# Performance work log

Measured on AMD Instinct MI355X. Metric: run time of the kernel, lower is better.

Reference implementation:

```python
import jax, jax.numpy as jnp
import numpy as np

QW, KW = 64, 128          # atom query / key window sizes
PAD = (KW - QW) // 2      # halo on each side of the key window
DEPTH, HEADS = 3, 4

def ln(x):
    m = jnp.mean(x, -1, keepdims=True)
    v = jnp.var(x, -1, keepdims=True)
    return (x - m) * jax.lax.rsqrt(v + 1e-5)

def q_windows(x):
    # x: (B, N, ...) -> (B, n, QW, ...); N assumed multiple of QW
    B, N = x.shape[0], x.shape[1]
    n = N // QW
    return x.reshape((B, n, QW) + x.shape[2:])

def k_windows(x):
    # x: (B, N, ...) -> (B, n, KW, ...) sliding key windows with zero halo padding
    B, N = x.shape[0], x.shape[1]
    n = N // QW
    pad_cfg = [(0, 0), (PAD, n * QW + PAD - N)] + [(0, 0)] * (x.ndim - 2)
    xp = jnp.pad(x, pad_cfg)
    idx = jnp.arange(n)[:, None] * QW + jnp.arange(KW)[None, :]
    return xp[:, idx]


def setup_inputs() -> dict:
    key = jax.random.key(0)
    ks = jax.random.split(key, 24)
    B, N, DS, DP, DT, NT = 2, 8192, 128, 16, 384, 1024
    w = lambda k, shp: (jax.random.normal(k, shp, jnp.float32) / np.sqrt(shp[-2])).astype(jnp.float32)
    inp = {
        'ref_pos': jax.random.normal(ks[0], (B, N, 3), jnp.float32),
        'ref_charge': jax.random.normal(ks[1], (B, N, 1), jnp.float32),
        'ref_mask': jnp.ones((B, N, 1), jnp.float32),
        'ref_element': jax.random.uniform(ks[2], (B, N, 128), jnp.float32),
        'ref_atom_name_chars': jax.random.uniform(ks[3], (B, N, 256), jnp.float32),
        'W_single': w(ks[4], (389, DS)),
        'W_pair': w(ks[5], (5, DP)),
        'W_outer': w(ks[6], (DS, 2 * DP)),
        'Wp_ff1': w(ks[7], (DP, 4 * DP)),
        'Wp_ff2': w(ks[8], (4 * DP, DP)),
        'Wq': w(ks[9], (DEPTH, DS, DS)),
        'Wk': w(ks[10], (DEPTH, DS, DS)),
        'Wv': w(ks[11], (DEPTH, DS, DS)),
        'Wo': w(ks[12], (DEPTH, DS, DS)),
        'Wb': w(ks[13], (DP, HEADS)),
        'Wff1': w(ks[14], (DEPTH, DS, 4 * DS)),
        'Wff2': w(ks[15], (DEPTH, 4 * DS, DS)),
        'W_out': w(ks[16], (DS, DT)),
        'ref_space_uid': jnp.sort(jax.random.randint(ks[17], (B, N), 0, NT), axis=-1),
        'atom_to_token_idx': jnp.sort(jax.random.randint(ks[18], (B, N), 0, NT), axis=-1),
        'n_tokens': NT,
    }
    return inp


def reference(ref_pos, ref_charge, ref_mask, ref_element, ref_atom_name_chars,
              W_single, W_pair, W_outer, Wp_ff1, Wp_ff2,
              Wq, Wk, Wv, Wo, Wb, Wff1, Wff2, W_out,
              ref_space_uid, atom_to_token_idx, n_tokens):
    B, N, _ = ref_pos.shape
    n = N // QW
    feats = jnp.concatenate([ref_pos, ref_charge, ref_mask, ref_element, ref_atom_name_chars], -1)
    s = feats @ W_single                                    # (B,N,DS) atom single repr

    # windowed pairwise geometric features
    pos_i, pos_j = q_windows(ref_pos), k_windows(ref_pos)   # (B,n,QW,3), (B,n,KW,3)
    uid_i, uid_j = q_windows(ref_space_uid), k_windows(ref_space_uid)
    dij = pos_i[:, :, :, None, :] - pos_j[:, :, None, :, :]  # (B,n,QW,KW,3)
    inv = 1.0 / (1.0 + jnp.sum(dij * dij, -1, keepdims=True))
    bij = (uid_i[:, :, :, None] == uid_j[:, :, None, :])
    pf = jnp.concatenate([dij, inv, bij[..., None].astype(dij.dtype)], -1)  # (...,5)
    pair = (pf @ W_pair) * bij[..., None].astype(dij.dtype)  # (B,n,QW,KW,DP)

    # pairwise outer-add from relu(single): Linear(DS->2*DP) split into i/j halves
    p = jax.nn.relu(s) @ W_outer
    DP = pair.shape[-1]
    pi, pj = p[..., :DP], p[..., DP:]
    pair = pair + q_windows(pi)[:, :, :, None, :] + k_windows(pj)[:, :, None, :, :]
    pair = pair + jax.nn.relu(ln(pair) @ Wp_ff1) @ Wp_ff2    # pair FF (residual)
    bias = jnp.einsum('bnqkc,ch->bnhqk', pair, Wb)           # attn pair bias

    # key validity mask for the halo-padded positions
    kidx = jnp.arange(n)[:, None] * QW + jnp.arange(KW)[None, :] - PAD
    kmask = jnp.where((kidx >= 0) & (kidx < N), 0.0, -1e9).astype(s.dtype)  # (n,KW)

    dh = s.shape[-1] // HEADS
    x = s
    for l in range(DEPTH):
        h = ln(x)
        q = q_windows(h @ Wq[l]).reshape(B, n, QW, HEADS, dh)
        k = k_windows(h @ Wk[l]).reshape(B, n, KW, HEADS, dh)
        v = k_windows(h @ Wv[l]).reshape(B, n, KW, HEADS, dh)
        logits = jnp.einsum('bnqhd,bnkhd->bnhqk', q, k) / np.sqrt(dh)
        logits = logits + bias + kmask[None, :, None, None, :]
        a = jax.nn.softmax(logits, -1)
        o = jnp.einsum('bnhqk,bnkhd->bnqhd', a, v).reshape(B, N, -1) @ Wo[l]
        x = x + o
        x = x + jax.nn.relu(ln(x) @ Wff1[l]) @ Wff2[l]

    tok = jax.nn.relu(x @ W_out)                             # (B,N,DT)

    def seg_mean(src, idx_):
        ssum = jax.ops.segment_sum(src, idx_, num_segments=n_tokens)
        cnt = jax.ops.segment_sum(jnp.ones((src.shape[0],), src.dtype), idx_, num_segments=n_tokens)
        return ssum / jnp.clip(cnt, 1.0)[:, None]

    return jax.vmap(seg_mean)(tok, atom_to_token_idx)        # (B, n_tokens, DT)
```

## Files before the change

kernel.cpp:

```cpp
#include <hip/hip_runtime.h>
#include <hip/hip_bf16.h>

#define QW 64
#define KW 128
#define PADW 32
#define DEPTH 3
#define HEADS 4
#define B_ 2
#define N_ 8192
#define DS 128
#define DP 16
#define DT 384
#define NT 1024
#define NWIN (N_ / QW)
#define DH (DS / HEADS)

typedef unsigned short u16;
typedef __attribute__((ext_vector_type(8))) short short8;
typedef __attribute__((ext_vector_type(4))) float f32x4v;
typedef __attribute__((ext_vector_type(4))) unsigned short us4;
typedef __attribute__((ext_vector_type(2))) short s16x2;

__device__ __forceinline__ u16 f2b(float x) {
    union { float f; unsigned u; } v; v.f = x;
    unsigned r = v.u + 0x7fffu + ((v.u >> 16) & 1u);
    return (u16)(r >> 16);
}
__device__ __forceinline__ float b2f(u16 h) {
    union { unsigned u; float f; } v; v.u = ((unsigned)h) << 16; return v.f;
}
__device__ __forceinline__ unsigned f2b2(float a, float b) {
    __hip_bfloat162 h = __float22bfloat162_rn(make_float2(a, b));
    union { __hip_bfloat162 h; unsigned u; } c; c.h = h; return c.u;
}
__device__ __forceinline__ us4 pack4(float a, float b, float c, float d) {
    union { us4 v; unsigned u[2]; } o;
    o.u[0] = f2b2(a, b);
    o.u[1] = f2b2(c, d);
    return o.v;
}
__device__ __forceinline__ us4 pack4_relu(float a, float b, float c, float d) {
    union { us4 v; s16x2 s[2]; unsigned u[2]; } o;
    o.u[0] = f2b2(a, b);
    o.u[1] = f2b2(c, d);
    o.s[0] = __builtin_elementwise_max(o.s[0], (s16x2)0);
    o.s[1] = __builtin_elementwise_max(o.s[1], (s16x2)0);
    return o.v;
}

template <int CTRL>
__device__ __forceinline__ float fdpp(float x) {
    int r = __builtin_amdgcn_update_dpp(0, __builtin_bit_cast(int, x),
                                        CTRL, 0xF, 0xF, true);
    return __builtin_bit_cast(float, r);
}
__device__ __forceinline__ float sum4_dpp(float x) {
    x += fdpp<0xB1>(x);
    x += fdpp<0x4E>(x);
    return x;
}
__device__ __forceinline__ float sum16_dpp(float x) {
    x += fdpp<0xB1>(x);
    x += fdpp<0x4E>(x);
    x += fdpp<0x124>(x);
    x += fdpp<0x128>(x);
    return x;
}
__device__ __forceinline__ float max16_dpp(float x) {
    x = fmaxf(x, fdpp<0xB1>(x));
    x = fmaxf(x, fdpp<0x4E>(x));
    x = fmaxf(x, fdpp<0x124>(x));
    x = fmaxf(x, fdpp<0x128>(x));
    return x;
}

__global__ __launch_bounds__(256) void convw_kernel(
    const float* __restrict__ Wq, const float* __restrict__ Wk,
    const float* __restrict__ Wv, const float* __restrict__ Wo,
    const float* __restrict__ Wff1, const float* __restrict__ Wff2,
    const float* __restrict__ Wout, const float* __restrict__ Wpff1,
    const float* __restrict__ Wpff2, const float* __restrict__ Wb,
    const float* __restrict__ Wsingle, const float* __restrict__ Wouter,
    u16* __restrict__ qkvT, u16* __restrict__ woT, u16* __restrict__ ff1T,
    u16* __restrict__ ff2T, u16* __restrict__ woutT,
    u16* __restrict__ w1T32, u16* __restrict__ wcatT,
    u16* __restrict__ wsT, u16* __restrict__ woutrT)
{
    int idx = blockIdx.x * 256 + threadIdx.x;
    if (idx < 3 * 384 * 128) {
        int l = idx / (384 * 128), r = idx % (384 * 128);
        int n = r / 128, k = r % 128;
        const float* W = (n < 128) ? Wq : (n < 256) ? Wk : Wv;
        qkvT[idx] = f2b(W[(size_t)l * 16384 + k * 128 + (n & 127)]);
    }
    if (idx < 3 * 128 * 128) {
        int l = idx / 16384, r = idx % 16384;
        int n = r / 128, k = r % 128;
        woT[idx] = f2b(Wo[(size_t)l * 16384 + k * 128 + n]);
    }
    if (idx < 3 * 512 * 128) {
        int l = idx / 65536, r = idx % 65536;
        int n = r / 128, k = r % 128;
        ff1T[idx] = f2b(Wff1[(size_t)l * 65536 + k * 512 + n]);
    }
    if (idx < 3 * 128 * 512) {
        int l = idx / 65536, r = idx % 65536;
        int n = r / 512, k = r % 512;
        ff2T[idx] = f2b(Wff2[(size_t)l * 65536 + k * 128 + n]);
    }
    if (idx < 384 * 128) {
        int n = idx / 128, k = idx % 128;
        woutT[idx] = f2b(Wout[(size_t)k * 384 + n]);
    }
    if (idx < 64 * 32) {
        int n = idx >> 5, k = idx & 31;
        w1T32[idx] = (k < 16) ? f2b(Wpff1[k * 64 + n]) : (u16)0;
    }
    if (idx < 16 * 96) {
        int h = idx / 96, k = idx % 96;
        float s = 0.f;
        if (h < 4) {
            if (k < 16) s = Wb[k * 4 + h];
            else if (k < 80) {
                int j = k - 16;
                for (int c = 0; c < 16; ++c) s += Wpff2[j * 16 + c] * Wb[c * 4 + h];
            }
        }
        wcatT[idx] = f2b(s);
    }
    if (idx < 128 * 416) {
        int n = idx / 416, k = idx % 416;
        float v = 0.f;
        if (k < 128)       v = Wsingle[(5 + k) * 128 + n];
        else if (k < 384)  v = Wsingle[(133 + k - 128) * 128 + n];
        else if (k < 387)  v = Wsingle[(k - 384) * 128 + n];
        else if (k == 387) v = Wsingle[3 * 128 + n];
        else if (k == 388) v = Wsingle[4 * 128 + n];
        wsT[idx] = f2b(v);
    }
    if (idx < 32 * 128) {
        int n = idx >> 7, k = idx & 127;
        woutrT[idx] = f2b(Wouter[k * 32 + n]);
    }
}

__global__ __launch_bounds__(256) void embed_gemm(
    const float* __restrict__ pos, const float* __restrict__ charge,
    const float* __restrict__ mask, const float* __restrict__ elem,
    const float* __restrict__ chars, const u16* __restrict__ wsT,
    const u16* __restrict__ woutrT, const u16* __restrict__ qkv0T,
    float* __restrict__ X, float* __restrict__ P, u16* __restrict__ QKVb)
{
    __shared__ __align__(16) u16 As[64 * 424];
    __shared__ float redS[64][4];
    const int LNOFF = 64 * 136;
    int tid = threadIdx.x;
    int row0 = blockIdx.x * 64;

    #pragma unroll
    for (int it = 0; it < 8; ++it) {
        int idx = tid + it * 256;
        int r = idx >> 5, c4 = idx & 31;
        f32x4v v = *(const f32x4v*)(elem + (size_t)(row0 + r) * 128 + c4 * 4);
        *(us4*)&As[r * 424 + c4 * 4] = pack4(v[0], v[1], v[2], v[3]);
    }
    #pragma unroll
    for (int it = 0; it < 16; ++it) {
        int idx = tid + it * 256;
        int r = idx >> 6, c4 = idx & 63;
        f32x4v v = *(const f32x4v*)(chars + (size_t)(row0 + r) * 256 + c4 * 4);
        *(us4*)&As[r * 424 + 128 + c4 * 4] = pack4(v[0], v[1], v[2], v[3]);
    }
    if (tid < 64) {
        int g = row0 + tid;
        As[tid * 424 + 384] = f2b(pos[g * 3]);
        As[tid * 424 + 385] = f2b(pos[g * 3 + 1]);
        As[tid * 424 + 386] = f2b(pos[g * 3 + 2]);
        As[tid * 424 + 387] = f2b(charge[g]);
        As[tid * 424 + 388] = f2b(mask[g]);
        for (int c = 389; c < 416; ++c) As[tid * 424 + c] = 0;
    }
    __syncthreads();

    int wv = tid >> 6, lane = tid & 63, quad = lane >> 4, l16 = lane & 15;
    int wm = (wv & 1) * 32, wn = (wv >> 1) * 64;
    f32x4v acc[2][4];
    #pragma unroll
    for (int i = 0; i < 2; ++i)
        #pragma unroll
        for (int j = 0; j < 4; ++j) acc[i][j] = (f32x4v){0.f, 0.f, 0.f, 0.f};

    #pragma unroll
    for (int kk = 0; kk < 13; ++kk) {
        short8 a0 = *(short8*)&As[(wm + l16) * 424 + kk * 32 + quad * 8];
        short8 a1 = *(short8*)&As[(wm + 16 + l16) * 424 + kk * 32 + quad * 8];
        #pragma unroll
        for (int nt = 0; nt < 4; ++nt) {
            short8 bw = *(const short8*)&wsT[(size_t)(wn + nt * 16 + l16) * 416 +
                                             kk * 32 + quad * 8];
            acc[0][nt] = __builtin_amdgcn_mfma_f32_16x16x32_bf16(a0, bw, acc[0][nt], 0, 0, 0);
            acc[1][nt] = __builtin_amdgcn_mfma_f32_16x16x32_bf16(a1, bw, acc[1][nt], 0, 0, 0);
        }
    }
    __syncthreads();

    #pragma unroll
    for (int mt = 0; mt < 2; ++mt) {
        #pragma unroll
        for (int r = 0; r < 4; ++r) {
            int lrow = wm + mt * 16 + quad * 4 + r;
            int row = row0 + lrow;
            float s = 0.f, ss = 0.f;
            #pragma unroll
            for (int nt = 0; nt < 4; ++nt) {
                float v = acc[mt][nt][r];
                int col = wn + nt * 16 + l16;
                X[(size_t)row * DS + col] = v;
                As[lrow * 136 + col] = f2b(fmaxf(v, 0.f));
                s += v; ss += v * v;
            }
            s  = sum16_dpp(s);
            ss = sum16_dpp(ss);
            if (l16 == 0) {
                redS[lrow][(wv >> 1) * 2]     = s;
                redS[lrow][(wv >> 1) * 2 + 1] = ss;
            }
        }
    }
    __syncthreads();

    #pragma unroll
    for (int mt = 0; mt < 2; ++mt)
        #pragma unroll
        for (int r = 0; r < 4; ++r) {
            int lrow = wm + mt * 16 + quad * 4 + r;
            f32x4v rv = *(f32x4v*)&redS[lrow][0];
            float s = rv[0] + rv[2], ss = rv[1] + rv[3];
            float m = s * (1.f / 128.f);
            float var = ss * (1.f / 128.f) - m * m;
            float rs = __builtin_amdgcn_rsqf(var + 1e-5f);
            #pragma unroll
            for (int nt = 0; nt < 4; ++nt) {
                int col = wn + nt * 16 + l16;
                As[LNOFF + lrow * 136 + col] = f2b((acc[mt][nt][r] - m) * rs);
            }
        }

    {
        f32x4v pacc[2];
        pacc[0] = (f32x4v){0.f, 0.f, 0.f, 0.f};
        pacc[1] = (f32x4v){0.f, 0.f, 0.f, 0.f};
        #pragma unroll
        for (int ks = 0; ks < 4; ++ks) {
            short8 a = *(short8*)&As[(wv * 16 + l16) * 136 + ks * 32 + quad * 8];
            #pragma unroll
            for (int nt = 0; nt < 2; ++nt) {
                short8 bw = *(const short8*)&woutrT[(size_t)(nt * 16 + l16) * 128 +
                                                    ks * 32 + quad * 8];
                pacc[nt] = __builtin_amdgcn_mfma_f32_16x16x32_bf16(a, bw, pacc[nt], 0, 0, 0);
            }
        }
        #pragma unroll
        for (int nt = 0; nt < 2; ++nt)
            #pragma unroll
            for (int r = 0; r < 4; ++r) {
                int row = row0 + wv * 16 + quad * 4 + r;
                P[(size_t)row * 32 + nt * 16 + l16] = pacc[nt][r];
            }
    }
    __syncthreads();

    for (int c = 0; c < 3; ++c) {
        int n0c = c * 128;
        f32x4v qa[2][4];
        #pragma unroll
        for (int i = 0; i < 2; ++i)
            #pragma unroll
            for (int j = 0; j < 4; ++j) qa[i][j] = (f32x4v){0.f, 0.f, 0.f, 0.f};
        #pragma unroll
        for (int ks = 0; ks < 4; ++ks) {
            short8 a0 = *(short8*)&As[LNOFF + (wm + l16) * 136 + ks * 32 + quad * 8];
            short8 a1 = *(short8*)&As[LNOFF + (wm + 16 + l16) * 136 + ks * 32 + quad * 8];
            #pragma unroll
            for (int nt = 0; nt < 4; ++nt) {
                short8 bw = *(const short8*)&qkv0T[(size_t)(n0c + wn + nt * 16 + l16) * 128 +
                                                   ks * 32 + quad * 8];
                qa[0][nt] = __builtin_amdgcn_mfma_f32_16x16x32_bf16(a0, bw, qa[0][nt], 0, 0, 0);
                qa[1][nt] = __builtin_amdgcn_mfma_f32_16x16x32_bf16(a1, bw, qa[1][nt], 0, 0, 0);
            }
        }
        #pragma unroll
        for (int mt = 0; mt < 2; ++mt)
            #pragma unroll
            for (int nt = 0; nt < 4; ++nt)
                #pragma unroll
                for (int r = 0; r < 4; ++r) {
                    int row = row0 + wm + mt * 16 + quad * 4 + r;
                    int col = n0c + wn + nt * 16 + l16;
                    QKVb[(size_t)row * 384 + col] = f2b(qa[mt][nt][r]);
                }
    }
}

__global__ __launch_bounds__(256) void bias_kernel(
    const float* __restrict__ pos, const int* __restrict__ uid,
    const float* __restrict__ P, const float* __restrict__ Wpair,
    const u16* __restrict__ w1T32, const u16* __restrict__ wcatT,
    u16* __restrict__ BIASb)
{
    __shared__ __align__(16) float posjS[128][4];
    __shared__ __align__(16) u16 lpS[4][16 * 24];
    __shared__ __align__(16) u16 A2S[4][16 * 104];

    int tid = threadIdx.x;
    int b  = blockIdx.x >> 11;
    int w  = (blockIdx.x >> 4) & 127;
    int qg = blockIdx.x & 15;

    if (tid < 128) {
        int r = tid;
        int jk = w * QW + r - PADW;
        bool valid = (jk >= 0) && (jk < N_);
        int gk = b * N_ + jk;
        float x = 0.f, y = 0.f, zz = 0.f; int u = 0;
        if (valid) { x = pos[gk * 3]; y = pos[gk * 3 + 1]; zz = pos[gk * 3 + 2]; u = uid[gk]; }
        posjS[r][0] = x; posjS[r][1] = y; posjS[r][2] = zz;
        ((int*)posjS[r])[3] = u;
    }

    int wv = tid >> 6, lane = tid & 63, quad = lane >> 4, l16 = lane & 15;
    int cl = lane >> 2, cg = lane & 3;
    int q = qg * 4 + wv;
    int gq = b * N_ + w * QW + q;

    float xi = pos[gq * 3], yi = pos[gq * 3 + 1], zi = pos[gq * 3 + 2];
    int ui = uid[gq];
    f32x4v pi4 = *(const f32x4v*)(P + (size_t)gq * 32 + cg * 4);
    f32x4v wp[5];
    #pragma unroll
    for (int f = 0; f < 5; ++f)
        wp[f] = *(const f32x4v*)(Wpair + f * 16 + cg * 4);
    short8 w1f[4], wcat[3];
    #pragma unroll
    for (int nt = 0; nt < 4; ++nt)
        w1f[nt] = *(const short8*)&w1T32[(nt * 16 + l16) * 32 + quad * 8];
    #pragma unroll
    for (int ks = 0; ks < 3; ++ks)
        wcat[ks] = *(const short8*)&wcatT[l16 * 96 + ks * 32 + quad * 8];

    f32x4v pjv[8];
    #pragma unroll
    for (int t = 0; t < 8; ++t) {
        int jk = w * QW + t * 16 + cl - PADW;
        bool valid = (jk >= 0) && (jk < N_);
        int gk = b * N_ + jk;
        f32x4v v = (f32x4v){0.f, 0.f, 0.f, 0.f};
        if (valid) v = *(const f32x4v*)(P + (size_t)gk * 32 + 16 + cg * 4);
        pjv[t] = v;
    }

    *(us4*)&A2S[wv][l16 * 104 + 80 + quad * 4] = (us4){0, 0, 0, 0};
    __syncthreads();

    size_t bbase = ((size_t)(b * NWIN + w) * HEADS) * (QW * KW);
    const short8 zero8 = (short8){0, 0, 0, 0, 0, 0, 0, 0};

    #pragma unroll 2
    for (int t = 0; t < 8; ++t) {
        int kk1 = t * 16 + cl;
        f32x4v pj4 = *(const f32x4v*)&posjS[kk1][0];
        float xj = pj4[0], yj = pj4[1], zj = pj4[2];
        int uj = __float_as_int(pj4[3]);
        float dx = xi - xj, dy = yi - yj, dz = zi - zj;
        float inv = __builtin_amdgcn_rcpf(1.f + dx * dx + dy * dy + dz * dz);
        float bf = (ui == uj) ? 1.f : 0.f;
        float pr[4];
        #pragma unroll
        for (int j = 0; j < 4; ++j) {
            float s = fmaf(dx, wp[0][j], fmaf(dy, wp[1][j],
                      fmaf(dz, wp[2][j], fmaf(inv, wp[3][j], wp[4][j]))));
            pr[j] = fmaf(bf, s, pi4[j] + pjv[t][j]);
        }
        float sum = pr[0] + pr[1] + pr[2] + pr[3];
        sum = sum4_dpp(sum);
        float m = sum * (1.f / 16.f);
        float d0 = pr[0] - m, d1 = pr[1] - m, d2 = pr[2] - m, d3 = pr[3] - m;
        float vs = d0 * d0 + d1 * d1 + d2 * d2 + d3 * d3;
        vs = sum4_dpp(vs);
        float rstd = __builtin_amdgcn_rsqf(vs * (1.f / 16.f) + 1e-5f);
        *(us4*)&lpS[wv][cl * 24 + cg * 4] =
            pack4(d0 * rstd, d1 * rstd, d2 * rstd, d3 * rstd);
        *(us4*)&A2S[wv][cl * 104 + cg * 4] = pack4(pr[0], pr[1], pr[2], pr[3]);

        short8 blp = zero8;
        if (quad < 2) blp = *(short8*)&lpS[wv][l16 * 24 + quad * 8];
        #pragma unroll
        for (int nt = 0; nt < 4; ++nt) {
            f32x4v z4 = (f32x4v){0.f, 0.f, 0.f, 0.f};
            z4 = __builtin_amdgcn_mfma_f32_16x16x32_bf16(w1f[nt], blp, z4, 0, 0, 0);
            *(us4*)&A2S[wv][l16 * 104 + 16 + nt * 16 + quad * 4] =
                pack4_relu(z4[0], z4[1], z4[2], z4[3]);
        }
        f32x4v acc = (f32x4v){0.f, 0.f, 0.f, 0.f};
        #pragma unroll
        for (int ks = 0; ks < 3; ++ks) {
            short8 a2 = *(short8*)&A2S[wv][l16 * 104 + ks * 32 + quad * 8];
            acc = __builtin_amdgcn_mfma_f32_16x16x32_bf16(a2, wcat[ks], acc, 0, 0, 0);
        }
        if (l16 < 4) {
            *(us4*)&BIASb[bbase + (size_t)l16 * (QW * KW) + q * KW +
                          t * 16 + quad * 4] = pack4(acc[0], acc[1], acc[2], acc[3]);
        }
    }
}

template <bool LAST>
__global__ __launch_bounds__(256) void wo_ff_fused(
    const u16* __restrict__ Ob, const u16* __restrict__ woT,
    const u16* __restrict__ w1T, const u16* __restrict__ w2T,
    const u16* __restrict__ auxT, float* __restrict__ X,
    u16* __restrict__ OutB)
{
    __shared__ __align__(16) u16 As[16 * 136];
    __shared__ __align__(16) u16 Hs[16 * 520];
    __shared__ __align__(16) float redS[16][8];
    int tid = threadIdx.x;
    int row0 = blockIdx.x * 16;
    int wv = tid >> 6, lane = tid & 63, quad = lane >> 4, l16 = lane & 15;
    int wn = wv * 32;

    int sr = tid >> 4, sc8 = tid & 15;
    short8 obv = *(const short8*)&Ob[(size_t)(row0 + sr) * 128 + sc8 * 8];
    float xres[2][4];
    #pragma unroll
    for (int nt = 0; nt < 2; ++nt)
        #pragma unroll
        for (int r = 0; r < 4; ++r)
            xres[nt][r] = X[(size_t)(row0 + quad * 4 + r) * DS + wn + nt * 16 + l16];
    short8 wow[2][4];
    #pragma unroll
    for (int nt = 0; nt < 2; ++nt)
        #pragma unroll
        for (int ks = 0; ks < 4; ++ks)
            wow[nt][ks] = *(const short8*)&woT[(size_t)(wn + nt * 16 + l16) * 128 +
                                               ks * 32 + quad * 8];

    *(short8*)&As[sr * 136 + sc8 * 8] = obv;
    __syncthreads();

    f32x4v acc[2];
    acc[0] = (f32x4v){0.f, 0.f, 0.f, 0.f};
    acc[1] = (f32x4v){0.f, 0.f, 0.f, 0.f};
    #pragma unroll
    for (int ks = 0; ks < 4; ++ks) {
        short8 a = *(short8*)&As[l16 * 136 + ks * 32 + quad * 8];
        acc[0] = __builtin_amdgcn_mfma_f32_16x16x32_bf16(a, wow[0][ks], acc[0], 0, 0, 0);
        acc[1] = __builtin_amdgcn_mfma_f32_16x16x32_bf16(a, wow[1][ks], acc[1], 0, 0, 0);
    }

    #pragma unroll
    for (int r = 0; r < 4; ++r) {
        int lrow = quad * 4 + r;
        float s = 0.f, ss = 0.f;
        #pragma unroll
        for (int nt = 0; nt < 2; ++nt) {
            float v = acc[nt][r] + xres[nt][r];
            acc[nt][r] = v;
            s += v; ss += v * v;
        }
        s  = sum16_dpp(s);
        ss = sum16_dpp(ss);
        if (l16 == 0) {
            redS[lrow][wv * 2]     = s;
            redS[lrow][wv * 2 + 1] = ss;
        }
    }
    short8 w1r[2][4];
    #pragma unroll
    for (int ks = 0; ks < 4; ++ks)
        w1r[0][ks] = *(const short8*)&w1T[(size_t)(wv * 128 + l16) * 128 +
                                          ks * 32 + quad * 8];
    __syncthreads();

    #pragma unroll
    for (int r = 0; r < 4; ++r) {
        int lrow = quad * 4 + r;
        f32x4v rv0 = *(f32x4v*)&redS[lrow][0];
        f32x4v rv1 = *(f32x4v*)&redS[lrow][4];
        float s  = rv0[0] + rv0[2] + rv1[0] + rv1[2];
        float ss = rv0[1] + rv0[3] + rv1[1] + rv1[3];
        float m = s * (1.f / 128.f);
        float var = ss * (1.f / 128.f) - m * m;
        float rs = __builtin_amdgcn_rsqf(var + 1e-5f);
        #pragma unroll
        for (int nt = 0; nt < 2; ++nt) {
            int col = wn + nt * 16 + l16;
            As[lrow * 136 + col] = f2b((acc[nt][r] - m) * rs);
        }
    }
    __syncthreads();

    {
        short8 brow[4];
        #pragma unroll
        for (int ks = 0; ks < 4; ++ks)
            brow[ks] = *(short8*)&As[l16 * 136 + ks * 32 + quad * 8];
        #pragma unroll
        for (int mt = 0; mt < 8; ++mt) {
            if (mt < 7) {
                #pragma unroll
                for (int ks = 0; ks < 4; ++ks)
                    w1r[(mt + 1) & 1][ks] =
                        *(const short8*)&w1T[(size_t)(wv * 128 + (mt + 1) * 16 + l16) * 128 +
                                             ks * 32 + quad * 8];
            }
            f32x4v c0 = (f32x4v){0.f, 0.f, 0.f, 0.f};
            #pragma unroll
            for (int ks = 0; ks < 4; ++ks)
                c0 = __builtin_amdgcn_mfma_f32_16x16x32_bf16(w1r[mt & 1][ks], brow[ks], c0, 0, 0, 0);
            *(us4*)&Hs[l16 * 520 + wv * 128 + mt * 16 + quad * 4] =
                pack4_relu(c0[0], c0[1], c0[2], c0[3]);
        }
    }
    short8 w2r[2][4];
    #pragma unroll
    for (int ksl = 0; ksl < 2; ++ksl)
        #pragma unroll
        for (int nt = 0; nt < 2; ++nt)
            w2r[0][ksl * 2 + nt] =
                *(const short8*)&w2T[(size_t)(wn + nt * 16 + l16) * 512 +
                                     ksl * 32 + quad * 8];
    __syncthreads();

    f32x4v acc2[2];
    acc2[0] = (f32x4v){0.f, 0.f, 0.f, 0.f};
    acc2[1] = (f32x4v){0.f, 0.f, 0.f, 0.f};
    #pragma unroll
    for (int cc = 0; cc < 8; ++cc) {
        if (cc < 7) {
            #pragma unroll
            for (int ksl = 0; ksl < 2; ++ksl)
                #pragma unroll
                for (int nt = 0; nt < 2; ++nt)
                    w2r[(cc + 1) & 1][ksl * 2 + nt] =
                        *(const short8*)&w2T[(size_t)(wn + nt * 16 + l16) * 512 +
                                             ((cc + 1) * 2 + ksl) * 32 + quad * 8];
        }
        #pragma unroll
        for (int ksl = 0; ksl < 2; ++ksl) {
            int ks = cc * 2 + ksl;
            short8 a = *(short8*)&Hs[l16 * 520 + ks * 32 + quad * 8];
            acc2[0] = __builtin_amdgcn_mfma_f32_16x16x32_bf16(a, w2r[cc & 1][ksl * 2 + 0], acc2[0], 0, 0, 0);
            acc2[1] = __builtin_amdgcn_mfma_f32_16x16x32_bf16(a, w2r[cc & 1][ksl * 2 + 1], acc2[1], 0, 0, 0);
        }
    }

    #pragma unroll
    for (int r = 0; r < 4; ++r) {
        int lrow = quad * 4 + r;
        int row = row0 + lrow;
        float s = 0.f, ss = 0.f;
        #pragma unroll
        for (int nt = 0; nt < 2; ++nt) {
            int col = wn + nt * 16 + l16;
            float v = acc2[nt][r] + acc[nt][r];
            acc2[nt][r] = v;
            X[(size_t)row * DS + col] = v;
            s += v; ss += v * v;
        }
        s  = sum16_dpp(s);
        ss = sum16_dpp(ss);
        if (l16 == 0) {
            redS[lrow][wv * 2]     = s;
            redS[lrow][wv * 2 + 1] = ss;
        }
    }
    short8 axr[2][4];
    #pragma unroll
    for (int ks = 0; ks < 4; ++ks)
        axr[0][ks] = *(const short8*)&auxT[(size_t)(wn + l16) * 128 +
                                           ks * 32 + quad * 8];
    __syncthreads();

    #pragma unroll
    for (int r = 0; r < 4; ++r) {
        int lrow = quad * 4 + r;
        float m = 0.f, rs = 1.f;
        if (!LAST) {
            f32x4v rv0 = *(f32x4v*)&redS[lrow][0];
            f32x4v rv1 = *(f32x4v*)&redS[lrow][4];
            float s  = rv0[0] + rv0[2] + rv1[0] + rv1[2];
            float ss = rv0[1] + rv0[3] + rv1[1] + rv1[3];
            m = s * (1.f / 128.f);
            float var = ss * (1.f / 128.f) - m * m;
            rs = __builtin_amdgcn_rsqf(var + 1e-5f);
        }
        #pragma unroll
        for (int nt = 0; nt < 2; ++nt) {
            int col = wn + nt * 16 + l16;
            float v = acc2[nt][r];
            As[lrow * 136 + col] = f2b(LAST ? v : (v - m) * rs);
        }
    }
    __syncthreads();

    {
        short8 arow[4];
        #pragma unroll
        for (int ks = 0; ks < 4; ++ks)
            arow[ks] = *(short8*)&As[l16 * 136 + ks * 32 + quad * 8];
        #pragma unroll
        for (int u = 0; u < 6; ++u) {
            if (u < 5) {
                int c1 = (u + 1) >> 1, n1 = (u + 1) & 1;
                #pragma unroll
                for (int ks = 0; ks < 4; ++ks)
                    axr[(u + 1) & 1][ks] =
                        *(const short8*)&auxT[(size_t)(c1 * 128 + wn + n1 * 16 + l16) * 128 +
                                              ks * 32 + quad * 8];
            }
            f32x4v qa = (f32x4v){0.f, 0.f, 0.f, 0.f};
            #pragma unroll
            for (int ks = 0; ks < 4; ++ks)
                qa = __builtin_amdgcn_mfma_f32_16x16x32_bf16(arow[ks], axr[u & 1][ks], qa, 0, 0, 0);
            int c = u >> 1, nt = u & 1;
            int col = c * 128 + wn + nt * 16 + l16;
            #pragma unroll
            for (int r = 0; r < 4; ++r) {
                float v = qa[r];
                if (LAST) v = fmaxf(v, 0.f);
                OutB[(size_t)(row0 + quad * 4 + r) * 384 + col] = f2b(v);
            }
        }
    }
}

__global__ __launch_bounds__(256) void attn_kernel(
    const u16* __restrict__ QKV, const u16* __restrict__ BIASb,
    u16* __restrict__ O)
{
    __shared__ __align__(16) u16 sQ[64 * 40];
    __shared__ __align__(16) u16 sK[128 * 40];
    __shared__ __align__(16) u16 sVt[32 * 152];
    __shared__ __align__(16) u16 sP[64 * 136];

    int tid = threadIdx.x;
    int h = blockIdx.x & 3, w = (blockIdx.x >> 2) & 127, b = blockIdx.x >> 9;
    size_t rowbase = (size_t)b * N_ + w * QW;
    size_t bbase = ((size_t)(b * NWIN + w) * HEADS + h) * (QW * KW);
    const short8 zero8 = (short8){0, 0, 0, 0, 0, 0, 0, 0};
    const bool edge = (w == 0) || (w == NWIN - 1);

    {
        int r = tid >> 2, d8 = (tid & 3) * 8;
        *(short8*)&sQ[r * 40 + d8] =
            *(const short8*)&QKV[(rowbase + r) * 384 + h * DH + d8];
    }
    #pragma unroll
    for (int i = 0; i < 2; ++i) {
        int idx = tid + i * 256;
        int r = idx >> 2, d8 = (idx & 3) * 8;
        int jk = w * QW + r - PADW;
        short8 v = zero8;
        if (jk >= 0 && jk < N_)
            v = *(const short8*)&QKV[((size_t)b * N_ + jk) * 384 + 128 + h * DH + d8];
        *(short8*)&sK[r * 40 + d8] = v;
    }
    {
        int kk = tid >> 1, d0 = (tid & 1) * 16;
        int jk = w * QW + kk - PADW;
        short8 v0 = zero8, v1 = zero8;
        if (jk >= 0 && jk < N_) {
            const u16* src = &QKV[((size_t)b * N_ + jk) * 384 + 256 + h * DH + d0];
            v0 = *(const short8*)src;
            v1 = *(const short8*)(src + 8);
        }
        #pragma unroll
        for (int j = 0; j < 8; ++j) {
            sVt[(d0 + j) * 152 + kk] = (u16)v0[j];
            sVt[(d0 + 8 + j) * 152 + kk] = (u16)v1[j];
        }
    }
    #pragma unroll
    for (int i = 0; i < 4; ++i) {
        int idx = tid + i * 256;
        int q = idx >> 4, c8 = idx & 15;
        *(short8*)&sP[q * 136 + c8 * 8] =
            *(const short8*)&BIASb[bbase + (size_t)q * KW + c8 * 8];
    }
    __syncthreads();

    int wv = tid >> 6, lane = tid & 63, quad = lane >> 4, l16 = lane & 15;
    const float scale = 0.17677669529663687f;

    short8 aq = *(short8*)&sQ[(wv * 16 + l16) * 40 + quad * 8];
    float e[8][4];
    #pragma unroll
    for (int nt = 0; nt < 8; ++nt) {
        short8 bk = *(short8*)&sK[(nt * 16 + l16) * 40 + quad * 8];
        f32x4v acc = (f32x4v){0.f, 0.f, 0.f, 0.f};
        acc = __builtin_amdgcn_mfma_f32_16x16x32_bf16(aq, bk, acc, 0, 0, 0);
        int kk = nt * 16 + l16;
        float msk = 0.f;
        if (edge) {
            int jk = w * QW + kk - PADW;
            msk = (jk >= 0 && jk < N_) ? 0.f : -1e9f;
        }
        #pragma unroll
        for (int r = 0; r < 4; ++r) {
            int q = wv * 16 + quad * 4 + r;
            e[nt][r] = acc[r] * scale + b2f(sP[q * 136 + kk]) + msk;
        }
    }

    #pragma unroll
    for (int r = 0; r < 4; ++r) {
        float m = e[0][r];
        #pragma unroll
        for (int nt = 1; nt < 8; ++nt) m = fmaxf(m, e[nt][r]);
        m = max16_dpp(m);
        float s = 0.f;
        #pragma unroll
        for (int nt = 0; nt < 8; ++nt) {
            float ev = __expf(e[nt][r] - m);
            e[nt][r] = ev;
            s += ev;
        }
        s = sum16_dpp(s);
        float inv = __builtin_amdgcn_rcpf(s);
        #pragma unroll
        for (int nt = 0; nt < 8; ++nt) e[nt][r] *= inv;
    }

    #pragma unroll
    for (int nt = 0; nt < 8; ++nt) {
        int kk = nt * 16 + l16;
        #pragma unroll
        for (int r = 0; r < 4; ++r) {
            int q = wv * 16 + quad * 4 + r;
            sP[q * 136 + kk] = f2b(e[nt][r]);
        }
    }

    short8 ap[4];
    #pragma unroll
    for (int ks = 0; ks < 4; ++ks)
        ap[ks] = *(short8*)&sP[(wv * 16 + l16) * 136 + ks * 32 + quad * 8];
    #pragma unroll
    for (int nt = 0; nt < 2; ++nt) {
        f32x4v acc = (f32x4v){0.f, 0.f, 0.f, 0.f};
        #pragma unroll
        for (int ks = 0; ks < 4; ++ks) {
            short8 bv = *(short8*)&sVt[(nt * 16 + l16) * 152 + ks * 32 + quad * 8];
            acc = __builtin_amdgcn_mfma_f32_16x16x32_bf16(ap[ks], bv, acc, 0, 0, 0);
        }
        int d = nt * 16 + l16;
        #pragma unroll
        for (int r = 0; r < 4; ++r) {
            int q = wv * 16 + quad * 4 + r;
            O[(rowbase + q) * DS + h * DH + d] = f2b(acc[r]);
        }
    }
}

__global__ __launch_bounds__(128) void seg_kernel(
    const u16* __restrict__ TOKb, const int* __restrict__ idx,
    float* __restrict__ out)
{
    int t = blockIdx.x & (NT - 1);
    int b = blockIdx.x >> 10;
    const int* id = idx + (size_t)b * N_;

    int lo = 0, hi = N_;
    while (lo < hi) { int mid = (lo + hi) >> 1; if (id[mid] < t) lo = mid + 1; else hi = mid; }
    int start = lo;
    hi = N_;
    while (lo < hi) { int mid = (lo + hi) >> 1; if (id[mid] < t + 1) lo = mid + 1; else hi = mid; }
    int end = lo;

    float inv = 1.f / fmaxf((float)(end - start), 1.f);
    if (threadIdx.x < 96) {
        int c4 = threadIdx.x * 4;
        f32x4v s = (f32x4v){0.f, 0.f, 0.f, 0.f};
        for (int r = start; r < end; ++r) {
            us4 v = *(const us4*)&TOKb[((size_t)b * N_ + r) * DT + c4];
            s[0] += b2f(v[0]); s[1] += b2f(v[1]);
            s[2] += b2f(v[2]); s[3] += b2f(v[3]);
        }
        s[0] *= inv; s[1] *= inv; s[2] *= inv; s[3] *= inv;
        *(f32x4v*)&out[((size_t)b * NT + t) * DT + c4] = s;
    }
}

extern "C" void kernel_launch(void* const* d_in, const int* in_sizes, int n_in,
                              void* d_out, int out_size, void* d_ws, size_t ws_size,
                              hipStream_t stream)
{
    const float* ref_pos    = (const float*)d_in[0];
    const float* ref_charge = (const float*)d_in[1];
    const float* ref_mask   = (const float*)d_in[2];
    const float* ref_elem   = (const float*)d_in[3];
    const float* ref_chars  = (const float*)d_in[4];
    const float* W_single   = (const float*)d_in[5];
    const float* W_pair     = (const float*)d_in[6];
    const float* W_outer    = (const float*)d_in[7];
    const float* Wp_ff1     = (const float*)d_in[8];
    const float* Wp_ff2     = (const float*)d_in[9];
    const float* Wq         = (const float*)d_in[10];
    const float* Wk         = (const float*)d_in[11];
    const float* Wv         = (const float*)d_in[12];
    const float* Wo         = (const float*)d_in[13];
    const float* Wb         = (const float*)d_in[14];
    const float* Wff1       = (const float*)d_in[15];
    const float* Wff2       = (const float*)d_in[16];
    const float* W_out      = (const float*)d_in[17];
    const int*   uid        = (const int*)d_in[18];
    const int*   a2t        = (const int*)d_in[19];
    float* out = (float*)d_out;

    const size_t ROWS = (size_t)B_ * N_;
    float* ws = (float*)d_ws;
    float* X    = ws;
    float* P    = X + ROWS * DS;
    u16* QKVb   = (u16*)(P + ROWS * 32);
    u16* Ob     = QKVb + ROWS * 384;
    u16* FFb    = Ob + ROWS * DS;
    u16* BIASb  = FFb + ROWS * 512;
    u16* TOKb   = BIASb + (size_t)B_ * NWIN * HEADS * QW * KW;
    u16* LNb    = TOKb + ROWS * DT;
    u16* qkvT   = LNb + ROWS * DS;
    u16* woT    = qkvT + 3 * 384 * 128;
    u16* ff1T   = woT + 3 * 128 * 128;
    u16* ff2T   = ff1T + 3 * 512 * 128;
    u16* woutT  = ff2T + 3 * 128 * 512;
    u16* w1T32  = woutT + 384 * 128;
    u16* wcatT  = w1T32 + 64 * 32;
    u16* wsT    = wcatT + 16 * 96;
    u16* woutrT = wsT + 128 * 416;

    convw_kernel<<<768, 256, 0, stream>>>(Wq, Wk, Wv, Wo, Wff1, Wff2, W_out,
                                          Wp_ff1, Wp_ff2, Wb, W_single, W_outer,
                                          qkvT, woT, ff1T, ff2T, woutT,
                                          w1T32, wcatT, wsT, woutrT);
    embed_gemm<<<ROWS / 64, 256, 0, stream>>>(ref_pos, ref_charge, ref_mask,
                                              ref_elem, ref_chars, wsT, woutrT,
                                              qkvT, X, P, QKVb);
    bias_kernel<<<4096, 256, 0, stream>>>(ref_pos, uid, P, W_pair,
                                          w1T32, wcatT, BIASb);

    for (int l = 0; l < DEPTH; ++l) {
        attn_kernel<<<B_ * NWIN * HEADS, 256, 0, stream>>>(QKVb, BIASb, Ob);
        if (l < DEPTH - 1) {
            wo_ff_fused<false><<<ROWS / 16, 256, 0, stream>>>(
                Ob, woT + (size_t)l * 128 * 128,
                ff1T + (size_t)l * 512 * 128, ff2T + (size_t)l * 128 * 512,
                qkvT + (size_t)(l + 1) * 384 * 128, X, QKVb);
        } else {
            wo_ff_fused<true><<<ROWS / 16, 256, 0, stream>>>(
                Ob, woT + (size_t)l * 128 * 128,
                ff1T + (size_t)l * 512 * 128, ff2T + (size_t)l * 128 * 512,
                woutT, X, TOKb);
        }
    }

    seg_kernel<<<B_ * NT, 128, 0, stream>>>(TOKb, a2t, out);
}
```

Measured before the change: 368.5 us.

## Batch weight fragment loads into two groups before MFMA in fused FFN kernel

Replaces the per-tile double-buffered global weight loads in the FF1, FF2 and aux projection stages with two large batches of loads issued up front, fenced by sched_barrier. All weight fragments are then in flight together before the MFMA chains start, which is meant to hide global memory latency better than prefetching one tile ahead. The cost is many more live VGPRs (up to 32 short8 per stage), which may reduce occupancy or cause spills.

```diff
diff --git a/kernel.cpp b/kernel.cpp
--- a/kernel.cpp
+++ b/kernel.cpp
@@ -444,7 +444,7 @@
         for (int ks = 0; ks < 4; ++ks)
             wow[nt][ks] = *(const short8*)&woT[(size_t)(wn + nt * 16 + l16) * 128 +
                                                ks * 32 + quad * 8];
-
+    __builtin_amdgcn_sched_barrier(0);
     *(short8*)&As[sr * 136 + sc8 * 8] = obv;
     __syncthreads();
 
@@ -475,11 +475,6 @@
             redS[lrow][wv * 2 + 1] = ss;
         }
     }
-    short8 w1r[2][4];
-    #pragma unroll
-    for (int ks = 0; ks < 4; ++ks)
-        w1r[0][ks] = *(const short8*)&w1T[(size_t)(wv * 128 + l16) * 128 +
-                                          ks * 32 + quad * 8];
     __syncthreads();
 
     #pragma unroll
@@ -505,53 +500,73 @@
         #pragma unroll
         for (int ks = 0; ks < 4; ++ks)
             brow[ks] = *(short8*)&As[l16 * 136 + ks * 32 + quad * 8];
-        #pragma unroll
-        for (int mt = 0; mt < 8; ++mt) {
-            if (mt < 7) {
-                #pragma unroll
-                for (int ks = 0; ks < 4; ++ks)
-                    w1r[(mt + 1) & 1][ks] =
-                        *(const short8*)&w1T[(size_t)(wv * 128 + (mt + 1) * 16 + l16) * 128 +
-                                             ks * 32 + quad * 8];
-            }
+
+        short8 wg0[4][4], wg1[4][4];
+        #pragma unroll
+        for (int t = 0; t < 4; ++t)
+            #pragma unroll
+            for (int ks = 0; ks < 4; ++ks)
+                wg0[t][ks] = *(const short8*)&w1T[(size_t)(wv * 128 + t * 16 + l16) * 128 +
+                                                  ks * 32 + quad * 8];
+        __builtin_amdgcn_sched_barrier(0);
+        #pragma unroll
+        for (int t = 0; t < 4; ++t)
+            #pragma unroll
+            for (int ks = 0; ks < 4; ++ks)
+                wg1[t][ks] = *(const short8*)&w1T[(size_t)(wv * 128 + (4 + t) * 16 + l16) * 128 +
+                                                  ks * 32 + quad * 8];
+        __builtin_amdgcn_sched_barrier(0);
+        #pragma unroll
+        for (int t = 0; t < 4; ++t) {
             f32x4v c0 = (f32x4v){0.f, 0.f, 0.f, 0.f};
             #pragma unroll
             for (int ks = 0; ks < 4; ++ks)
-                c0 = __builtin_amdgcn_mfma_f32_16x16x32_bf16(w1r[mt & 1][ks], brow[ks], c0, 0, 0, 0);
-            *(us4*)&Hs[l16 * 520 + wv * 128 + mt * 16 + quad * 4] =
+                c0 = __builtin_amdgcn_mfma_f32_16x16x32_bf16(wg0[t][ks], brow[ks], c0, 0, 0, 0);
+            *(us4*)&Hs[l16 * 520 + wv * 128 + t * 16 + quad * 4] =
                 pack4_relu(c0[0], c0[1], c0[2], c0[3]);
         }
-    }
-    short8 w2r[2][4];
-    #pragma unroll
-    for (int ksl = 0; ksl < 2; ++ksl)
-        #pragma unroll
-        for (int nt = 0; nt < 2; ++nt)
-            w2r[0][ksl * 2 + nt] =
-                *(const short8*)&w2T[(size_t)(wn + nt * 16 + l16) * 512 +
-                                     ksl * 32 + quad * 8];
+        #pragma unroll
+        for (int t = 0; t < 4; ++t) {
+            f32x4v c0 = (f32x4v){0.f, 0.f, 0.f, 0.f};
+            #pragma unroll
+            for (int ks = 0; ks < 4; ++ks)
+                c0 = __builtin_amdgcn_mfma_f32_16x16x32_bf16(wg1[t][ks], brow[ks], c0, 0, 0, 0);
+            *(us4*)&Hs[l16 * 520 + wv * 128 + (4 + t) * 16 + quad * 4] =
+                pack4_relu(c0[0], c0[1], c0[2], c0[3]);
+        }
+    }
     __syncthreads();
 
     f32x4v acc2[2];
     acc2[0] = (f32x4v){0.f, 0.f, 0.f, 0.f};
     acc2[1] = (f32x4v){0.f, 0.f, 0.f, 0.f};
-    #pragma unroll
-    for (int cc = 0; cc < 8; ++cc) {
-        if (cc < 7) {
-            #pragma unroll
-            for (int ksl = 0; ksl < 2; ++ksl)
-                #pragma unroll
-                for (int nt = 0; nt < 2; ++nt)
-                    w2r[(cc + 1) & 1][ksl * 2 + nt] =
-                        *(const short8*)&w2T[(size_t)(wn + nt * 16 + l16) * 512 +
-                                             ((cc + 1) * 2 + ksl) * 32 + quad * 8];
-        }
-        #pragma unroll
-        for (int ksl = 0; ksl < 2; ++ksl) {
-            int ks = cc * 2 + ksl;
-            short8 a = *(short8*)&Hs[l16 * 520 + ks * 32 + quad * 8];
-            acc2[0] = __builtin_amdgcn_mfma_f32_16x16x32_bf16(a, w2r[cc & 1][ksl * 2 + 0], acc2[0], 0, 0, 0);
-            acc2[1] = __builtin_amdgcn_mfma_f32_16x16x32_bf16(a, w2r[cc & 1][ksl * 2 + 1], acc2[1], 0, 0, 0);
+    {
+        short8 w2g0[8][2], w2g1[8][2];
+        #pragma unroll
+        for (int k8 = 0; k8 < 8; ++k8)
+            #pragma unroll
+            for (int nt = 0; nt < 2; ++nt)
+                w2g0[k8][nt] = *(const short8*)&w2T[(size_t)(wn + nt * 16 + l16) * 512 +
+                                                    k8 * 32 + quad * 8];
+        __builtin_amdgcn_sched_barrier(0);
+        #pragma unroll
+        for (int k8 = 0; k8 < 8; ++k8)
+            #pragma unroll
+            for (int nt = 0; nt < 2; ++nt)
+                w2g1[k8][nt] = *(const short8*)&w2T[(size_t)(wn + nt * 16 + l16) * 512 +
+                                                    (8 + k8) * 32 + quad * 8];
+        __builtin_amdgcn_sched_barrier(0);
+        #pragma unroll
+        for (int k8 = 0; k8 < 8; ++k8) {
+            short8 a = *(short8*)&Hs[l16 * 520 + k8 * 32 + quad * 8];
+            acc2[0] = __builtin_amdgcn_mfma_f32_16x16x32_bf16(a, w2g0[k8][0], acc2[0], 0, 0, 0);
+            acc2[1] = __builtin_amdgcn_mfma_f32_16x16x32_bf16(a, w2g0[k8][1], acc2[1], 0, 0, 0);
+        }
+        #pragma unroll
+        for (int k8 = 0; k8 < 8; ++k8) {
+            short8 a = *(short8*)&Hs[l16 * 520 + (8 + k8) * 32 + quad * 8];
+            acc2[0] = __builtin_amdgcn_mfma_f32_16x16x32_bf16(a, w2g1[k8][0], acc2[0], 0, 0, 0);
+            acc2[1] = __builtin_amdgcn_mfma_f32_16x16x32_bf16(a, w2g1[k8][1], acc2[1], 0, 0, 0);
         }
     }
 
@@ -575,11 +590,6 @@
             redS[lrow][wv * 2 + 1] = ss;
         }
     }
-    short8 axr[2][4];
-    #pragma unroll
-    for (int ks = 0; ks < 4; ++ks)
-        axr[0][ks] = *(const short8*)&auxT[(size_t)(wn + l16) * 128 +
-                                           ks * 32 + quad * 8];
     __syncthreads();
 
     #pragma unroll
@@ -609,21 +619,48 @@
         #pragma unroll
         for (int ks = 0; ks < 4; ++ks)
             arow[ks] = *(short8*)&As[l16 * 136 + ks * 32 + quad * 8];
-        #pragma unroll
-        for (int u = 0; u < 6; ++u) {
-            if (u < 5) {
-                int c1 = (u + 1) >> 1, n1 = (u + 1) & 1;
-                #pragma unroll
-                for (int ks = 0; ks < 4; ++ks)
-                    axr[(u + 1) & 1][ks] =
-                        *(const short8*)&auxT[(size_t)(c1 * 128 + wn + n1 * 16 + l16) * 128 +
-                                              ks * 32 + quad * 8];
+
+        short8 axg0[3][4], axg1[3][4];
+        #pragma unroll
+        for (int t = 0; t < 3; ++t) {
+            int c = t >> 1, nt = t & 1;
+            #pragma unroll
+            for (int ks = 0; ks < 4; ++ks)
+                axg0[t][ks] = *(const short8*)&auxT[(size_t)(c * 128 + wn + nt * 16 + l16) * 128 +
+                                                    ks * 32 + quad * 8];
+        }
+        __builtin_amdgcn_sched_barrier(0);
+        #pragma unroll
+        for (int t = 0; t < 3; ++t) {
+            int u = 3 + t, c = u >> 1, nt = u & 1;
+            #pragma unroll
+            for (int ks = 0; ks < 4; ++ks)
+                axg1[t][ks] = *(const short8*)&auxT[(size_t)(c * 128 + wn + nt * 16 + l16) * 128 +
+                                                    ks * 32 + quad * 8];
+        }
+        __builtin_amdgcn_sched_barrier(0);
+        #pragma unroll
+        for (int t = 0; t < 3; ++t) {
+            f32x4v qa = (f32x4v){0.f, 0.f, 0.f, 0.f};
+            #pragma unroll
+            for (int ks = 0; ks < 4; ++ks)
+                qa = __builtin_amdgcn_mfma_f32_16x16x32_bf16(arow[ks], axg0[t][ks], qa, 0, 0, 0);
+            int c = t >> 1, nt = t & 1;
+            int col = c * 128 + wn + nt * 16 + l16;
+            #pragma unroll
+            for (int r = 0; r < 4; ++r) {
+                float v = qa[r];
+                if (LAST) v = fmaxf(v, 0.f);
+                OutB[(size_t)(row0 + quad * 4 + r) * 384 + col] = f2b(v);
             }
+        }
+        #pragma unroll
+        for (int t = 0; t < 3; ++t) {
             f32x4v qa = (f32x4v){0.f, 0.f, 0.f, 0.f};
             #pragma unroll
             for (int ks = 0; ks < 4; ++ks)
-                qa = __builtin_amdgcn_mfma_f32_16x16x32_bf16(arow[ks], axr[u & 1][ks], qa, 0, 0, 0);
-            int c = u >> 1, nt = u & 1;
+                qa = __builtin_amdgcn_mfma_f32_16x16x32_bf16(arow[ks], axg1[t][ks], qa, 0, 0, 0);
+            int u = 3 + t, c = u >> 1, nt = u & 1;
             int col = c * 128 + wn + nt * 16 + l16;
             #pragma unroll
             for (int r = 0; r < 4; ++r) {
```

Result: no change. 372.3 us (+1.0%).
